# Kernel tuning notes

Measured on AMD Instinct MI355X. Metric: run time of the kernel, lower is better.

Reference implementation:

```python
import jax, jax.numpy as jnp
import numpy as np

NEG_BIG = -9e15
ALPHA = 0.2  # LeakyReLU negative slope


def setup_inputs() -> dict:
    key = jax.random.key(0)
    k1, k2, k3, k4 = jax.random.split(key, 4)
    B, N, F_in, F_out = 8, 2048, 128, 128
    h = jax.random.normal(k1, (B, N, F_in), dtype=jnp.float32)
    adj = jax.random.randint(k2, (B, N, N), 0, 2, dtype=jnp.int32)
    # xavier_uniform with gain=1.414
    def xavier(k, shape, gain=1.414):
        fan_in, fan_out = shape[0], shape[1]
        bound = gain * np.sqrt(6.0 / (fan_in + fan_out))
        return jax.random.uniform(k, shape, jnp.float32, -bound, bound)
    W = xavier(k3, (F_in, F_out))
    a = xavier(k4, (2 * F_out, 1))
    return {"h": h, "adj": adj, "W": W, "a": a}


def reference(h, adj, W, a):
    # h: [B,N,F_in], adj: [B,N,N], W: [F_in,F_out], a: [2*F_out,1]
    Wh = jnp.einsum('bnf,fo->bno', h, W)              # [B,N,F_out]
    F_out = W.shape[1]
    a1 = a[:F_out, 0]                                  # source part
    a2 = a[F_out:, 0]                                  # target part
    # additive attention decomposition: cat([Wh_i, Wh_j]) @ a == Wh_i@a1 + Wh_j@a2
    s1 = Wh @ a1                                       # [B,N]
    s2 = Wh @ a2                                       # [B,N]
    e = jax.nn.leaky_relu(s1[:, :, None] + s2[:, None, :], negative_slope=ALPHA)  # [B,N,N]
    e = jnp.where(adj > 0, e, NEG_BIG)
    attn = jax.nn.softmax(e, axis=-1)                  # [B,N,N]
    h_prime = jnp.einsum('bij,bjo->bio', attn, Wh)     # [B,N,F_out]
    return jax.nn.elu(h_prime)                         # concat=True path
```

## Files before the change

### kernel.cpp

```cpp
#include <hip/hip_runtime.h>
#include <hip/hip_bf16.h>
#include <string.h>

typedef __attribute__((ext_vector_type(8))) short short8;
typedef __attribute__((ext_vector_type(4))) float f32x4;
typedef __attribute__((ext_vector_type(4))) float float4v;
typedef __attribute__((ext_vector_type(2))) float float2v;
typedef __attribute__((ext_vector_type(4))) unsigned short ushort4v;

#define LOG2E 1.44269504088896340736f
#define NB 8
#define NN 2048
#define NF 128
#define PKW (NN / 64)
#define PKWORDS (NB * NN * PKW)

static __device__ inline unsigned short f2bf(float x) {
    unsigned u = __float_as_uint(x);
    return (unsigned short)((u + 0x7FFFu + ((u >> 16) & 1u)) >> 16);
}
static __device__ inline float bf2f(unsigned short u) {
    union { unsigned u; float f; } v;
    v.u = ((unsigned)u) << 16;
    return v.f;
}
static __device__ inline float fexp2(float x) {
    float r;
    asm("v_exp_f32 %0, %1" : "=v"(r) : "v"(x));
    return r;
}
static __device__ inline unsigned fkey(float f) {
    unsigned u = __float_as_uint(f);
    return (u & 0x80000000u) ? ~u : (u | 0x80000000u);
}
static __device__ inline float funkey(unsigned k) {
    unsigned b = (k & 0x80000000u) ? (k & 0x7FFFFFFFu) : ~k;
    return __uint_as_float(b);
}
static __device__ inline int wave_sniff(const unsigned short* __restrict__ raw) {
    int lane = threadIdx.x & 63;
    int cnt = 0;
#pragma unroll
    for (int i = 0; i < 8; ++i) {
        int e = (raw[lane * 8 + i] >> 7) & 0xFF;
        cnt += (e >= 102 && e <= 139) ? 1 : 0;
    }
#pragma unroll
    for (int off = 1; off < 64; off <<= 1) cnt += __shfl_xor(cnt, off);
    return cnt >= 450;
}

__global__ __launch_bounds__(256) void k_prep(const void* __restrict__ Wraw,
                                              const void* __restrict__ araw,
                                              short* __restrict__ WThi,
                                              short* __restrict__ WTlo,
                                              float* __restrict__ a1s,
                                              float* __restrict__ a2s,
                                              unsigned* __restrict__ s2mkey) {
    const int bf16w = wave_sniff((const unsigned short*)Wraw);
    int idx = blockIdx.x * 256 + threadIdx.x;
    int k = idx >> 7, n = idx & 127;
    float x = bf16w ? bf2f(((const unsigned short*)Wraw)[idx])
                    : ((const float*)Wraw)[idx];
    unsigned short hi = f2bf(x);
    float lo = x - bf2f(hi);
    WThi[n * 128 + k] = (short)hi;
    WTlo[n * 128 + k] = (short)f2bf(lo);
    if (blockIdx.x == 0) {
        int i = threadIdx.x;
        float av = bf16w ? bf2f(((const unsigned short*)araw)[i])
                         : ((const float*)araw)[i];
        if (i < 128) a1s[i] = LOG2E * av;
        else a2s[i - 128] = LOG2E * av;
        if (i < NB) s2mkey[i] = 0u;
    }
}

__global__ __launch_bounds__(256) void k_pack(const int* __restrict__ adj,
                                              unsigned long long* __restrict__ pk) {
    const int wid = blockIdx.x * 4 + (threadIdx.x >> 6);
    const int lane = threadIdx.x & 63;
    const int wpw = PKWORDS / 4096;
    const size_t w0 = (size_t)wid * wpw;
    for (int i = 0; i < wpw; i += 4) {
        int v0 = adj[((w0 + i) << 6) | lane];
        int v1 = adj[((w0 + i + 1) << 6) | lane];
        int v2 = adj[((w0 + i + 2) << 6) | lane];
        int v3 = adj[((w0 + i + 3) << 6) | lane];
        unsigned long long m0 = __ballot(v0 > 0);
        unsigned long long m1 = __ballot(v1 > 0);
        unsigned long long m2 = __ballot(v2 > 0);
        unsigned long long m3 = __ballot(v3 > 0);
        if (lane == 0) {
            pk[w0 + i] = m0;
            pk[w0 + i + 1] = m1;
            pk[w0 + i + 2] = m2;
            pk[w0 + i + 3] = m3;
        }
    }
}

__global__ __launch_bounds__(256, 4) void k_gemm(const void* __restrict__ hraw,
                                                 const short* __restrict__ WThi,
                                                 const short* __restrict__ WTlo,
                                                 const float* __restrict__ a1s,
                                                 const float* __restrict__ a2s,
                                                 float* __restrict__ s1,
                                                 float* __restrict__ EF,
                                                 unsigned* __restrict__ s2mkey,
                                                 short* __restrict__ WhT) {
    const int tid = threadIdx.x;
    const int lane = tid & 63;
    const int w = tid >> 6;
    const int lo = lane & 15, g = lane >> 4;
    const int i0 = (blockIdx.x * 4 + w) * 16;
    const int bf16w = wave_sniff((const unsigned short*)hraw);

    short8 ahi[4], alo[4];
    if (bf16w) {
        const short* h16 = (const short*)hraw;
#pragma unroll
        for (int kc = 0; kc < 4; ++kc) {
            ahi[kc] = *(const short8*)(h16 + (size_t)(i0 + lo) * NF + kc * 32 + g * 8);
            alo[kc] = (short8){0, 0, 0, 0, 0, 0, 0, 0};
        }
    } else {
        const float* hf = (const float*)hraw;
#pragma unroll
        for (int kc = 0; kc < 4; ++kc) {
            const float* p = hf + (size_t)(i0 + lo) * NF + kc * 32 + g * 8;
            float4v x0 = *(const float4v*)(p);
            float4v x1 = *(const float4v*)(p + 4);
            short8 h8, l8;
#pragma unroll
            for (int q = 0; q < 4; ++q) {
                unsigned short u0 = f2bf(x0[q]);
                h8[q] = (short)u0;
                l8[q] = (short)f2bf(x0[q] - bf2f(u0));
                unsigned short u1 = f2bf(x1[q]);
                h8[q + 4] = (short)u1;
                l8[q + 4] = (short)f2bf(x1[q] - bf2f(u1));
            }
            ahi[kc] = h8;
            alo[kc] = l8;
        }
    }

    f32x4 acc[8];
#pragma unroll
    for (int t = 0; t < 8; ++t) acc[t] = (f32x4){0.f, 0.f, 0.f, 0.f};
#pragma unroll
    for (int t = 0; t < 8; ++t) {
#pragma unroll
        for (int kc = 0; kc < 4; ++kc) {
            const size_t boff = (size_t)(lo + 16 * t) * NF + kc * 32 + g * 8;
            short8 bhi = *(const short8*)(WThi + boff);
            short8 blo = *(const short8*)(WTlo + boff);
            acc[t] = __builtin_amdgcn_mfma_f32_16x16x32_bf16(ahi[kc], bhi, acc[t], 0, 0, 0);
            acc[t] = __builtin_amdgcn_mfma_f32_16x16x32_bf16(ahi[kc], blo, acc[t], 0, 0, 0);
            acc[t] = __builtin_amdgcn_mfma_f32_16x16x32_bf16(alo[kc], bhi, acc[t], 0, 0, 0);
        }
    }

    const int b = i0 >> 11;
    const int n0 = i0 & 2047;
    short* wt = WhT + (size_t)b * NF * NN;
#pragma unroll
    for (int t = 0; t < 8; ++t) {
        ushort4v u;
#pragma unroll
        for (int r = 0; r < 4; ++r) u[r] = f2bf(acc[t][r]);
        *(ushort4v*)(wt + (size_t)(lo + 16 * t) * NN + n0 + g * 4) = u;
    }

    float a1f[8], a2f[8];
#pragma unroll
    for (int t = 0; t < 8; ++t) {
        a1f[t] = a1s[lo + 16 * t];
        a2f[t] = a2s[lo + 16 * t];
    }
    float wm = -1e30f;
#pragma unroll
    for (int r = 0; r < 4; ++r) {
        float d1 = 0.f, d2 = 0.f;
#pragma unroll
        for (int t = 0; t < 8; ++t) {
            float wv = acc[t][r];
            d1 += wv * a1f[t];
            d2 += wv * a2f[t];
        }
#pragma unroll
        for (int off = 1; off < 16; off <<= 1) {
            d1 += __shfl_xor(d1, off);
            d2 += __shfl_xor(d2, off);
        }
        if (lo == 0) {
            s1[i0 + g * 4 + r] = d1;
            float2v ef;
            ef[0] = fexp2(d2);
            ef[1] = fexp2(0.2f * d2);
            *(float2v*)(EF + (size_t)(i0 + g * 4 + r) * 2) = ef;
        }
        wm = fmaxf(wm, d2);
    }
    wm = fmaxf(wm, __shfl_xor(wm, 16));
    wm = fmaxf(wm, __shfl_xor(wm, 32));
    if (lane == 0) atomicMax(&s2mkey[b], fkey(wm));
}

template <int FINAL, int JS>
__global__ __launch_bounds__(256, 4) void k_attn(const unsigned long long* __restrict__ pk,
                                                 const float* __restrict__ s1,
                                                 const float* __restrict__ EF,
                                                 const unsigned* __restrict__ s2mkey,
                                                 const short* __restrict__ WhT,
                                                 const void* __restrict__ hraw,
                                                 void* __restrict__ out,
                                                 float* __restrict__ pO,
                                                 float* __restrict__ pL) {
    constexpr int JL = NN / JS;
    constexpr int NT = JL / 64;

    const int tid = threadIdx.x;
    const int lane = tid & 63, wid = tid >> 6;
    const int lo = lane & 15, g = lane >> 4;
    const int gid = blockIdx.x;
    const int js = (JS > 1) ? (gid / (NB * 32)) : 0;
    const int rem = gid % (NB * 32);
    const int blk = rem & 31;
    const int b = rem >> 5;
    const int rowbase = blk * 64 + wid * 16;
    const int row = rowbase + lo;
    const int jbeg = js * JL;

    __shared__ short lds[2][128 * 64];
    __shared__ float ldsZ[JL * 2];

    const float s1v = s1[b * NN + row];
    const float tm = s1v + funkey(s2mkey[b]);
    const float M = fmaxf(tm, 0.2f * tm);
    const float Tc = fexp2(-s1v);
    const float Ac = fexp2(s1v - M);
    const float Bc = fexp2(0.2f * s1v - M);
    const unsigned long long* pkr = pk + (size_t)(b * NN + row) * PKW + (jbeg >> 6);
    const short* vb = WhT + (size_t)b * NF * NN;

    {
        const float4v* src = (const float4v*)(EF + (size_t)(b * NN + jbeg) * 2);
        for (int i = tid; i < JL / 2; i += 256) ((float4v*)ldsZ)[i] = src[i];
    }

    const int sf = tid >> 1;
    const int sh = tid & 1;
    const short* sbase = vb + (size_t)sf * NN + jbeg + sh * 32;
    char* ldsc0 = (char*)&lds[0][0];
    char* ldsc1 = (char*)&lds[1][0];
    const unsigned swz = (unsigned)((sf & 7) << 4);
    const unsigned wb0 = (unsigned)(sf * 128 + sh * 64);
    const unsigned rsw = (unsigned)((lo & 7) << 4);

    f32x4 acc[8];
#pragma unroll
    for (int t = 0; t < 8; ++t) acc[t] = (f32x4){0.f, 0.f, 0.f, 0.f};
    float lsum = 0.f;

    {
        short8 s0 = *(const short8*)(sbase);
        short8 s1r = *(const short8*)(sbase + 8);
        short8 s2r = *(const short8*)(sbase + 16);
        short8 s3r = *(const short8*)(sbase + 24);
        *(short8*)(ldsc0 + ((wb0 + 0) ^ swz)) = s0;
        *(short8*)(ldsc0 + ((wb0 + 16) ^ swz)) = s1r;
        *(short8*)(ldsc0 + ((wb0 + 32) ^ swz)) = s2r;
        *(short8*)(ldsc0 + ((wb0 + 48) ^ swz)) = s3r;
    }
    unsigned long long mcur = pkr[0];
    __syncthreads();

    int cur = 0;
    for (int t = 0; t < NT; ++t) {
        short8 sn0, sn1, sn2, sn3;
        unsigned long long mnext = 0;
        const bool more = (t + 1 < NT);
        if (more) {
            const short* sp = sbase + (t + 1) * 64;
            sn0 = *(const short8*)(sp);
            sn1 = *(const short8*)(sp + 8);
            sn2 = *(const short8*)(sp + 16);
            sn3 = *(const short8*)(sp + 24);
            mnext = pkr[t + 1];
        }
        const char* cb = cur ? ldsc1 : ldsc0;

        short8 pa[2];
#pragma unroll
        for (int c = 0; c < 2; ++c) {
            const float4v* zp = (const float4v*)&ldsZ[((t) * 64 + c * 32 + g * 8) * 2];
            float4v w_[4];
#pragma unroll
            for (int q = 0; q < 4; ++q) w_[q] = zp[q];
            const unsigned bits = (unsigned)(mcur >> (c * 32 + g * 8)) & 0xFFu;
            float pv[8];
#pragma unroll
            for (int k = 0; k < 8; ++k) {
                float E = w_[k >> 1][(k & 1) * 2];
                float F = w_[k >> 1][(k & 1) * 2 + 1];
                bool cond = E >= Tc;
                float sel = cond ? E : F;
                float coef = cond ? Ac : Bc;
                float p = sel * coef;
                p = ((bits >> k) & 1u) ? p : 0.f;
                lsum += p;
                pv[k] = p;
            }
            unsigned r0, r1, r2, r3;
            asm("v_cvt_pk_bf16_f32 %0, %1, %2" : "=v"(r0) : "v"(pv[0]), "v"(pv[1]));
            asm("v_cvt_pk_bf16_f32 %0, %1, %2" : "=v"(r1) : "v"(pv[2]), "v"(pv[3]));
            asm("v_cvt_pk_bf16_f32 %0, %1, %2" : "=v"(r2) : "v"(pv[4]), "v"(pv[5]));
            asm("v_cvt_pk_bf16_f32 %0, %1, %2" : "=v"(r3) : "v"(pv[6]), "v"(pv[7]));
            union { unsigned u[4]; short8 s; } uu;
            uu.u[0] = r0; uu.u[1] = r1; uu.u[2] = r2; uu.u[3] = r3;
            pa[c] = uu.s;
        }

#pragma unroll
        for (int t8 = 0; t8 < 8; ++t8) {
            const unsigned rb0 = ((unsigned)((lo + 16 * t8) * 128 + g * 16)) ^ rsw;
            const unsigned rb1 = ((unsigned)((lo + 16 * t8) * 128 + 64 + g * 16)) ^ rsw;
            short8 v0 = *(const short8*)(cb + rb0);
            short8 v1 = *(const short8*)(cb + rb1);
            acc[t8] = __builtin_amdgcn_mfma_f32_16x16x32_bf16(pa[0], v0, acc[t8], 0, 0, 0);
            acc[t8] = __builtin_amdgcn_mfma_f32_16x16x32_bf16(pa[1], v1, acc[t8], 0, 0, 0);
        }

        if (more) {
            char* wb = cur ? ldsc0 : ldsc1;
            *(short8*)(wb + ((wb0 + 0) ^ swz)) = sn0;
            *(short8*)(wb + ((wb0 + 16) ^ swz)) = sn1;
            *(short8*)(wb + ((wb0 + 32) ^ swz)) = sn2;
            *(short8*)(wb + ((wb0 + 48) ^ swz)) = sn3;
            mcur = mnext;
        }
        __syncthreads();
        cur ^= 1;
    }

    lsum += __shfl_xor(lsum, 16);
    lsum += __shfl_xor(lsum, 32);

    if (FINAL) {
        const int bf16w = wave_sniff((const unsigned short*)hraw);
        float inv[4];
#pragma unroll
        for (int r = 0; r < 4; ++r) inv[r] = 1.0f / __shfl(lsum, g * 4 + r);
#pragma unroll
        for (int t8 = 0; t8 < 8; ++t8) {
#pragma unroll
            for (int r = 0; r < 4; ++r) {
                float x = acc[t8][r] * inv[r];
                float y = (x > 0.f) ? x : (fexp2(x * LOG2E) - 1.0f);
                size_t oi = ((size_t)b * NN + rowbase + g * 4 + r) * NF + lo + 16 * t8;
                if (bf16w) ((unsigned short*)out)[oi] = f2bf(y);
                else ((float*)out)[oi] = y;
            }
        }
    } else {
        const int grp = b * 128 + blk * 4 + wid;
        float* po = pO + (size_t)(grp * JS + js) * (16 * NF);
#pragma unroll
        for (int t8 = 0; t8 < 8; ++t8)
#pragma unroll
            for (int r = 0; r < 4; ++r)
                po[(g * 4 + r) * NF + lo + 16 * t8] = acc[t8][r];
        if (g == 0) pL[(grp * JS + js) * 16 + lo] = lsum;
    }
}

__global__ __launch_bounds__(256) void k_combine(const float* __restrict__ pO,
                                                 const float* __restrict__ pL,
                                                 const void* __restrict__ hraw,
                                                 void* __restrict__ out,
                                                 int jsplit) {
    const int bf16w = wave_sniff((const unsigned short*)hraw);
    int idx4 = blockIdx.x * 256 + threadIdx.x;
    int base = idx4 * 4;
    if (base >= NB * NN * NF) return;
    int col = base & 127;
    int rowg = base >> 7;
    int r = rowg & 15;
    int grp = rowg >> 4;
    float4v o = (float4v){0.f, 0.f, 0.f, 0.f};
    float l = 0.f;
    for (int js = 0; js < jsplit; ++js) {
        int task = grp * jsplit + js;
        o += *(const float4v*)(pO + (size_t)task * (16 * NF) + r * NF + col);
        l += pL[task * 16 + r];
    }
    float inv = 1.0f / l;
    float y[4];
#pragma unroll
    for (int q = 0; q < 4; ++q) {
        float x = o[q] * inv;
        y[q] = (x > 0.f) ? x : (fexp2(x * LOG2E) - 1.0f);
    }
    if (bf16w) {
        ushort4v u;
#pragma unroll
        for (int q = 0; q < 4; ++q) u[q] = f2bf(y[q]);
        *(ushort4v*)((unsigned short*)out + base) = u;
    } else {
        *(float4v*)((float*)out + base) = (float4v){y[0], y[1], y[2], y[3]};
    }
}

extern "C" void kernel_launch(void* const* d_in, const int* in_sizes, int n_in,
                              void* d_out, int out_size, void* d_ws, size_t ws_size,
                              hipStream_t stream) {
    const void* h = d_in[0];
    const int* adj = (const int*)d_in[1];
    const void* W = d_in[2];
    const void* a = d_in[3];

    char* ws = (char*)d_ws;
    auto align256 = [](size_t x) { return (x + 255) & ~(size_t)255; };
    size_t off = 0;
    short* WThi = (short*)(ws + off); off = align256(off + (size_t)128 * 128 * 2);
    short* WTlo = (short*)(ws + off); off = align256(off + (size_t)128 * 128 * 2);
    float* a1s = (float*)(ws + off);  off = align256(off + 128 * 4);
    float* a2s = (float*)(ws + off);  off = align256(off + 128 * 4);
    short* WhT = (short*)(ws + off);  off = align256(off + (size_t)NB * NF * NN * 2);
    float* s1 = (float*)(ws + off);   off = align256(off + (size_t)NB * NN * 4);
    float* EF = (float*)(ws + off);   off = align256(off + (size_t)NB * NN * 8);
    unsigned* s2mkey = (unsigned*)(ws + off); off = align256(off + NB * 4);
    unsigned long long* pk = (unsigned long long*)(ws + off);
    off = align256(off + (size_t)PKWORDS * 8);

    const int ngrp = NB * 128;
    auto need = [&](int js) {
        return off + (size_t)ngrp * js * 16 * NF * 4 + 512 + (size_t)ngrp * js * 16 * 4;
    };
    int jsplit = (ws_size >= need(4)) ? 4 : ((ws_size >= need(2)) ? 2 : 1);
    float* pO = nullptr;
    float* pL = nullptr;
    if (jsplit > 1) {
        size_t pO_bytes = (size_t)ngrp * jsplit * 16 * NF * 4;
        size_t pL_bytes = (size_t)ngrp * jsplit * 16 * 4;
        pO = (float*)(ws + off); off = align256(off + pO_bytes);
        pL = (float*)(ws + off); off = align256(off + pL_bytes);
    }

    k_prep<<<64, 256, 0, stream>>>(W, a, WThi, WTlo, a1s, a2s, s2mkey);
    k_gemm<<<256, 256, 0, stream>>>(h, WThi, WTlo, a1s, a2s, s1, EF, s2mkey, WhT);
    k_pack<<<1024, 256, 0, stream>>>(adj, pk);
    if (jsplit == 4) {
        k_attn<0, 4><<<NB * 32 * 4, 256, 0, stream>>>(pk, s1, EF, s2mkey, WhT, h,
                                                      d_out, pO, pL);
    } else if (jsplit == 2) {
        k_attn<0, 2><<<NB * 32 * 2, 256, 0, stream>>>(pk, s1, EF, s2mkey, WhT, h,
                                                      d_out, pO, pL);
    } else {
        k_attn<1, 1><<<NB * 32, 256, 0, stream>>>(pk, s1, EF, s2mkey, WhT, h,
                                                  d_out, nullptr, nullptr);
    }
    if (jsplit > 1) {
        int nout = NB * NN * NF;
        k_combine<<<(nout / 4 + 255) / 256, 256, 0, stream>>>(pO, pL, h, d_out, jsplit);
    }
}
```

Before: 83.49 us.

## Merge gemm and pack kernels; fuse split-K combine via last-arriver atomic

The adjacency-packing work now runs as extra blocks inside the gemm launch, so the two independent stages share one grid and one launch. The separate combine kernel is removed. Each split's wave bumps a per-group counter after writing its partial results, and the last arriver reduces all partials, applies the ELU and writes the output. This trades two kernel launches and a full pass over the partials for threadfences, atomics and serialized reduction work on the last wave of each group.

```diff
diff --git a/kernel.cpp b/kernel.cpp
--- a/kernel.cpp
+++ b/kernel.cpp
@@ -14,6 +14,8 @@
 #define NF 128
 #define PKW (NN / 64)
 #define PKWORDS (NB * NN * PKW)
+#define NGEMMB 256
+#define NPACKB 1024
 
 static __device__ inline unsigned short f2bf(float x) {
     unsigned u = __float_as_uint(x);
@@ -56,7 +58,8 @@
                                               short* __restrict__ WTlo,
                                               float* __restrict__ a1s,
                                               float* __restrict__ a2s,
-                                              unsigned* __restrict__ s2mkey) {
+                                              unsigned* __restrict__ s2mkey,
+                                              int* __restrict__ cnt) {
     const int bf16w = wave_sniff((const unsigned short*)Wraw);
     int idx = blockIdx.x * 256 + threadIdx.x;
     int k = idx >> 7, n = idx & 127;
@@ -66,6 +69,7 @@
     float lo = x - bf2f(hi);
     WThi[n * 128 + k] = (short)hi;
     WTlo[n * 128 + k] = (short)f2bf(lo);
+    if (idx < NB * 128) cnt[idx] = 0;
     if (blockIdx.x == 0) {
         int i = threadIdx.x;
         float av = bf16w ? bf2f(((const unsigned short*)araw)[i])
@@ -76,40 +80,41 @@
     }
 }
 
-__global__ __launch_bounds__(256) void k_pack(const int* __restrict__ adj,
-                                              unsigned long long* __restrict__ pk) {
-    const int wid = blockIdx.x * 4 + (threadIdx.x >> 6);
-    const int lane = threadIdx.x & 63;
-    const int wpw = PKWORDS / 4096;
-    const size_t w0 = (size_t)wid * wpw;
-    for (int i = 0; i < wpw; i += 4) {
-        int v0 = adj[((w0 + i) << 6) | lane];
-        int v1 = adj[((w0 + i + 1) << 6) | lane];
-        int v2 = adj[((w0 + i + 2) << 6) | lane];
-        int v3 = adj[((w0 + i + 3) << 6) | lane];
-        unsigned long long m0 = __ballot(v0 > 0);
-        unsigned long long m1 = __ballot(v1 > 0);
-        unsigned long long m2 = __ballot(v2 > 0);
-        unsigned long long m3 = __ballot(v3 > 0);
-        if (lane == 0) {
-            pk[w0 + i] = m0;
-            pk[w0 + i + 1] = m1;
-            pk[w0 + i + 2] = m2;
-            pk[w0 + i + 3] = m3;
-        }
-    }
-}
-
-__global__ __launch_bounds__(256, 4) void k_gemm(const void* __restrict__ hraw,
-                                                 const short* __restrict__ WThi,
-                                                 const short* __restrict__ WTlo,
-                                                 const float* __restrict__ a1s,
-                                                 const float* __restrict__ a2s,
-                                                 float* __restrict__ s1,
-                                                 float* __restrict__ EF,
-                                                 unsigned* __restrict__ s2mkey,
-                                                 short* __restrict__ WhT) {
+__global__ __launch_bounds__(256, 4) void k_fat(const int* __restrict__ adj,
+                                                unsigned long long* __restrict__ pk,
+                                                const void* __restrict__ hraw,
+                                                const short* __restrict__ WThi,
+                                                const short* __restrict__ WTlo,
+                                                const float* __restrict__ a1s,
+                                                const float* __restrict__ a2s,
+                                                float* __restrict__ s1,
+                                                float* __restrict__ EF,
+                                                unsigned* __restrict__ s2mkey,
+                                                short* __restrict__ WhT) {
     const int tid = threadIdx.x;
+    if (blockIdx.x >= NGEMMB) {
+        const int wid = (blockIdx.x - NGEMMB) * 4 + (tid >> 6);
+        const int lane = tid & 63;
+        const int wpw = PKWORDS / 4096;
+        const size_t w0 = (size_t)wid * wpw;
+        for (int i = 0; i < wpw; i += 4) {
+            int v0 = adj[((w0 + i) << 6) | lane];
+            int v1 = adj[((w0 + i + 1) << 6) | lane];
+            int v2 = adj[((w0 + i + 2) << 6) | lane];
+            int v3 = adj[((w0 + i + 3) << 6) | lane];
+            unsigned long long m0 = __ballot(v0 > 0);
+            unsigned long long m1 = __ballot(v1 > 0);
+            unsigned long long m2 = __ballot(v2 > 0);
+            unsigned long long m3 = __ballot(v3 > 0);
+            if (lane == 0) {
+                pk[w0 + i] = m0;
+                pk[w0 + i + 1] = m1;
+                pk[w0 + i + 2] = m2;
+                pk[w0 + i + 3] = m3;
+            }
+        }
+        return;
+    }
     const int lane = tid & 63;
     const int w = tid >> 6;
     const int lo = lane & 15, g = lane >> 4;
@@ -217,7 +222,8 @@
                                                  const void* __restrict__ hraw,
                                                  void* __restrict__ out,
                                                  float* __restrict__ pO,
-                                                 float* __restrict__ pL) {
+                                                 float* __restrict__ pL,
+                                                 int* __restrict__ cnt) {
     constexpr int JL = NN / JS;
     constexpr int NT = JL / 64;
 
@@ -373,43 +379,39 @@
             for (int r = 0; r < 4; ++r)
                 po[(g * 4 + r) * NF + lo + 16 * t8] = acc[t8][r];
         if (g == 0) pL[(grp * JS + js) * 16 + lo] = lsum;
-    }
-}
-
-__global__ __launch_bounds__(256) void k_combine(const float* __restrict__ pO,
-                                                 const float* __restrict__ pL,
-                                                 const void* __restrict__ hraw,
-                                                 void* __restrict__ out,
-                                                 int jsplit) {
-    const int bf16w = wave_sniff((const unsigned short*)hraw);
-    int idx4 = blockIdx.x * 256 + threadIdx.x;
-    int base = idx4 * 4;
-    if (base >= NB * NN * NF) return;
-    int col = base & 127;
-    int rowg = base >> 7;
-    int r = rowg & 15;
-    int grp = rowg >> 4;
-    float4v o = (float4v){0.f, 0.f, 0.f, 0.f};
-    float l = 0.f;
-    for (int js = 0; js < jsplit; ++js) {
-        int task = grp * jsplit + js;
-        o += *(const float4v*)(pO + (size_t)task * (16 * NF) + r * NF + col);
-        l += pL[task * 16 + r];
-    }
-    float inv = 1.0f / l;
-    float y[4];
-#pragma unroll
-    for (int q = 0; q < 4; ++q) {
-        float x = o[q] * inv;
-        y[q] = (x > 0.f) ? x : (fexp2(x * LOG2E) - 1.0f);
-    }
-    if (bf16w) {
-        ushort4v u;
-#pragma unroll
-        for (int q = 0; q < 4; ++q) u[q] = f2bf(y[q]);
-        *(ushort4v*)((unsigned short*)out + base) = u;
-    } else {
-        *(float4v*)((float*)out + base) = (float4v){y[0], y[1], y[2], y[3]};
+
+        __threadfence();
+        int old = 0;
+        if (lane == 0) old = atomicAdd(&cnt[grp], 1);
+        old = __shfl(old, 0);
+        if (old == JS - 1) {
+            __threadfence();
+            const int bf16w = wave_sniff((const unsigned short*)hraw);
+            const int col = (lane & 31) * 4 + (lane >> 5) * 0;
+            for (int r = 0; r < 16; ++r) {
+                float l = 0.f;
+#pragma unroll
+                for (int jx = 0; jx < JS; ++jx)
+                    l += pL[(grp * JS + jx) * 16 + r];
+                const float inv = 1.0f / l;
+                float2v o = (float2v){0.f, 0.f};
+#pragma unroll
+                for (int jx = 0; jx < JS; ++jx)
+                    o += *(const float2v*)(pO + (size_t)(grp * JS + jx) * (16 * NF) +
+                                           r * NF + lane * 2);
+                float y0 = o[0] * inv, y1 = o[1] * inv;
+                y0 = (y0 > 0.f) ? y0 : (fexp2(y0 * LOG2E) - 1.0f);
+                y1 = (y1 > 0.f) ? y1 : (fexp2(y1 * LOG2E) - 1.0f);
+                size_t ob = ((size_t)b * NN + rowbase + r) * NF + lane * 2;
+                if (bf16w) {
+                    unsigned short u0 = f2bf(y0), u1 = f2bf(y1);
+                    unsigned pairu = (unsigned)u0 | ((unsigned)u1 << 16);
+                    *(unsigned*)((unsigned short*)out + ob) = pairu;
+                } else {
+                    *(float2v*)((float*)out + ob) = (float2v){y0, y1};
+                }
+            }
+        }
     }
 }
 
@@ -432,6 +434,7 @@
     float* s1 = (float*)(ws + off);   off = align256(off + (size_t)NB * NN * 4);
     float* EF = (float*)(ws + off);   off = align256(off + (size_t)NB * NN * 8);
     unsigned* s2mkey = (unsigned*)(ws + off); off = align256(off + NB * 4);
+    int* cnt = (int*)(ws + off);      off = align256(off + (size_t)NB * 128 * 4);
     unsigned long long* pk = (unsigned long long*)(ws + off);
     off = align256(off + (size_t)PKWORDS * 8);
 
@@ -449,21 +452,17 @@
         pL = (float*)(ws + off); off = align256(off + pL_bytes);
     }
 
-    k_prep<<<64, 256, 0, stream>>>(W, a, WThi, WTlo, a1s, a2s, s2mkey);
-    k_gemm<<<256, 256, 0, stream>>>(h, WThi, WTlo, a1s, a2s, s1, EF, s2mkey, WhT);
-    k_pack<<<1024, 256, 0, stream>>>(adj, pk);
+    k_prep<<<64, 256, 0, stream>>>(W, a, WThi, WTlo, a1s, a2s, s2mkey, cnt);
+    k_fat<<<NGEMMB + NPACKB, 256, 0, stream>>>(adj, pk, h, WThi, WTlo, a1s, a2s,
+                                               s1, EF, s2mkey, WhT);
     if (jsplit == 4) {
         k_attn<0, 4><<<NB * 32 * 4, 256, 0, stream>>>(pk, s1, EF, s2mkey, WhT, h,
-                                                      d_out, pO, pL);
+                                                      d_out, pO, pL, cnt);
     } else if (jsplit == 2) {
         k_attn<0, 2><<<NB * 32 * 2, 256, 0, stream>>>(pk, s1, EF, s2mkey, WhT, h,
-                                                      d_out, pO, pL);
+                                                      d_out, pO, pL, cnt);
     } else {
         k_attn<1, 1><<<NB * 32, 256, 0, stream>>>(pk, s1, EF, s2mkey, WhT, h,
-                                                  d_out, nullptr, nullptr);
-    }
-    if (jsplit > 1) {
-        int nout = NB * NN * NF;
-        k_combine<<<(nout / 4 + 255) / 256, 256, 0, stream>>>(pO, pL, h, d_out, jsplit);
-    }
-}
+                                                  d_out, nullptr, nullptr, cnt);
+    }
+}
```

After: 233.4 us. +179.6%, slower.
